# Kernel tuning notes

Hardware: AMD Instinct MI355X
Metric: run time of the kernel (lower is better)

Reference implementation:

```python
import jax, jax.numpy as jnp
import numpy as np

N_NODES = 100000
N_EDGES = 600000
D_IN = 128
D_OUT = 128

def gcn_conv(x, src, dst, W, b, n):
    # PyG GCNConv: h = X W; out_i = sum_j norm_ij * h_j + b, with self-loops and
    # symmetric normalization norm_ij = deg_i^{-1/2} deg_j^{-1/2}.
    deg = jax.ops.segment_sum(jnp.ones_like(dst, dtype=x.dtype), dst, num_segments=n)
    dinv = jnp.where(deg > 0, jax.lax.rsqrt(deg), 0.0)
    norm = dinv[src] * dinv[dst]            # [E]
    h = x @ W                                # [N, D_out]
    msg = h[src] * norm[:, None]             # gather + scale, [E, D_out]
    out = jax.ops.segment_sum(msg, dst, num_segments=n)
    return out + b

def setup_inputs() -> dict:
    key = jax.random.key(0)
    ks = jax.random.split(key, 8)
    x = jax.random.normal(ks[0], (N_NODES, D_IN), dtype=jnp.float32)
    edge_index = jax.random.randint(ks[1], (2, N_EDGES), 0, N_NODES, dtype=jnp.int64)
    s = (1.0 / np.sqrt(D_IN)).astype(np.float32) if isinstance(np.sqrt(D_IN), np.ndarray) else np.float32(1.0 / np.sqrt(D_IN))
    W1 = jax.random.normal(ks[2], (D_IN, D_OUT), dtype=jnp.float32) * s
    b1 = jnp.zeros((D_OUT,), dtype=jnp.float32)
    W2 = jax.random.normal(ks[3], (D_OUT, D_OUT), dtype=jnp.float32) * np.float32(1.0 / np.sqrt(D_OUT))
    b2 = jnp.zeros((D_OUT,), dtype=jnp.float32)
    Wfc = jax.random.normal(ks[4], (D_IN, D_OUT), dtype=jnp.float32) * s
    bfc = jnp.zeros((D_OUT,), dtype=jnp.float32)
    return {"x": x, "edge_index": edge_index, "W1": W1, "b1": b1,
            "W2": W2, "b2": b2, "Wfc": Wfc, "bfc": bfc}

def reference(x, edge_index, W1, b1, W2, b2, Wfc, bfc):
    n = x.shape[0]
    loop = jnp.arange(n, dtype=edge_index.dtype)
    src = jnp.concatenate([edge_index[0], loop])  # add self-loops
    dst = jnp.concatenate([edge_index[1], loop])
    res = x @ Wfc + bfc                           # linear residual branch
    h = jax.nn.relu(gcn_conv(x, src, dst, W1, b1, n))
    h = jax.nn.relu(gcn_conv(h, src, dst, W2, b2, n))
    return h + res
```

## Files before the change

### kernel.cpp

```cpp
#include <hip/hip_runtime.h>
#include <hip/hip_bf16.h>

#define D 128

typedef __bf16 bf16x8 __attribute__((ext_vector_type(8)));
typedef float f32x16 __attribute__((ext_vector_type(16)));

union U16 { uint4 u; bf16x8 v; };

static __device__ __forceinline__ unsigned short f2bf(float f) {
    unsigned u = __float_as_uint(f);
    unsigned r = (u + 0x7fffu + ((u >> 16) & 1u)) >> 16;
    return (unsigned short)r;
}
static __device__ __forceinline__ float bf2f(unsigned short s) {
    return __uint_as_float(((unsigned)s) << 16);
}
static __device__ __forceinline__ float u2f_lo(unsigned x) { return __uint_as_float(x << 16); }
static __device__ __forceinline__ float u2f_hi(unsigned x) { return __uint_as_float(x & 0xffff0000u); }

__global__ __launch_bounds__(256) void k_prep(
        const float* __restrict__ W1, const float* __restrict__ W2, const float* __restrict__ Wf,
        unsigned short* __restrict__ W1h, unsigned short* __restrict__ W1l,
        unsigned short* __restrict__ W2h, unsigned short* __restrict__ W2l,
        unsigned short* __restrict__ Wfh, unsigned short* __restrict__ Wfl,
        int* __restrict__ cnt, int n) {
    int idx = blockIdx.x * 256 + threadIdx.x;
    if (idx < 3 * 16384) {
        int which = idx >> 14;
        int local = idx & 16383;
        int k = local >> 7, c = local & 127;
        const float* W = (which == 0) ? W1 : (which == 1) ? W2 : Wf;
        unsigned short* Wh = (which == 0) ? W1h : (which == 1) ? W2h : Wfh;
        unsigned short* Wl = (which == 0) ? W1l : (which == 1) ? W2l : Wfl;
        float v = W[k * 128 + c];
        unsigned short h = f2bf(v);
        unsigned short l = f2bf(v - bf2f(h));
        Wh[c * 128 + k] = h;
        Wl[c * 128 + k] = l;
    }
    if (idx < n) cnt[idx] = 0;
}


__global__ __launch_bounds__(256) void k_hist(const int* __restrict__ dst,
                                              int* __restrict__ cnt, int e) {
    int i = blockIdx.x * 256 + threadIdx.x;
    if (i < e) atomicAdd(&cnt[dst[i]], 1);
}

#define SCAN_CHUNK 1024

__global__ __launch_bounds__(256) void k_scan_local(const int* __restrict__ cnt,
                                                    int* __restrict__ ptr,
                                                    int* __restrict__ sums, int n) {
    __shared__ int tsum[256];
    const int t = threadIdx.x;
    const int base = blockIdx.x * SCAN_CHUNK + t * 4;
    int v[4]; int s = 0;
    #pragma unroll
    for (int i = 0; i < 4; ++i) {
        int idx = base + i;
        v[i] = (idx < n) ? cnt[idx] : 0;
        s += v[i];
    }
    tsum[t] = s;
    __syncthreads();
    for (int off = 1; off < 256; off <<= 1) {
        int x = (t >= off) ? tsum[t - off] : 0;
        __syncthreads();
        tsum[t] += x;
        __syncthreads();
    }
    int run = (t > 0) ? tsum[t - 1] : 0;
    if (t == 255) sums[blockIdx.x] = tsum[255];
    #pragma unroll
    for (int i = 0; i < 4; ++i) {
        int idx = base + i;
        if (idx < n) ptr[idx] = run;
        run += v[i];
    }
}

__global__ __launch_bounds__(256) void k_scan_sums(int* __restrict__ sums, int nChunks) {
    __shared__ int ls[256];
    const int t = threadIdx.x;
    ls[t] = (t < nChunks) ? sums[t] : 0;
    __syncthreads();
    for (int off = 1; off < 256; off <<= 1) {
        int x = (t >= off) ? ls[t - off] : 0;
        __syncthreads();
        ls[t] += x;
        __syncthreads();
    }
    if (t < nChunks) sums[t] = (t > 0) ? ls[t - 1] : 0;
}

__global__ __launch_bounds__(256) void k_scan_add(int* __restrict__ ptr,
                                                  const int* __restrict__ sums,
                                                  int* __restrict__ cnt,
                                                  float* __restrict__ dinv,
                                                  int n, int e) {
    int i = blockIdx.x * 256 + threadIdx.x;
    if (i < n) {
        ptr[i] += sums[i >> 10];
        dinv[i] = rsqrtf((float)(1 + cnt[i]));
        cnt[i] = 0;
    }
    if (i == 0) ptr[n] = e;
}

__global__ __launch_bounds__(256) void k_fill(const int* __restrict__ src,
                                              const int* __restrict__ dst,
                                              const int* __restrict__ ptr,
                                              int* __restrict__ fill,
                                              int* __restrict__ csr_src, int e) {
    int i = blockIdx.x * 256 + threadIdx.x;
    if (i < e) {
        int d = dst[i];
        int slot = ptr[d] + atomicAdd(&fill[d], 1);
        csr_src[slot] = src[i];
    }
}

#define APAD 136

__global__ __launch_bounds__(256, 4) void k_gemm_rr(
        const float* __restrict__ A,
        const unsigned short* __restrict__ Bh, const unsigned short* __restrict__ Bl,
        const float* __restrict__ bias,
        unsigned short* __restrict__ outb,
        float* __restrict__ outf,
        int M, int nTiles) {
    __shared__ __align__(16) unsigned short As[2][32][APAD];

    const int tid = threadIdx.x;
    const int wave = tid >> 6;
    const int lane = tid & 63;
    const int l31 = lane & 31;
    const int quad8 = (lane >> 5) * 8;
    const int col = wave * 32 + l31;

    U16 bh[8], bl[8];
    #pragma unroll
    for (int ks = 0; ks < 8; ++ks) {
        const size_t bo = (size_t)col * D + ks * 16 + quad8;
        bh[ks].u = *(const uint4*)(Bh + bo);
        bl[ks].u = *(const uint4*)(Bl + bo);
    }
    const float bv = (bias != nullptr) ? bias[col] : 0.f;

    for (int t = blockIdx.x; t < nTiles; t += gridDim.x) {
        const int row0 = t * 32;

        #pragma unroll
        for (int i = 0; i < 4; ++i) {
            int f = tid + i * 256;
            int r = f >> 5, c4 = (f & 31) * 4;
            int rg = row0 + r; if (rg >= M) rg = M - 1;
            float4 v = *(const float4*)(A + (size_t)rg * D + c4);
            ushort4 hq, lq;
            hq.x = f2bf(v.x); hq.y = f2bf(v.y); hq.z = f2bf(v.z); hq.w = f2bf(v.w);
            lq.x = f2bf(v.x - bf2f(hq.x)); lq.y = f2bf(v.y - bf2f(hq.y));
            lq.z = f2bf(v.z - bf2f(hq.z)); lq.w = f2bf(v.w - bf2f(hq.w));
            *(ushort4*)&As[0][r][c4] = hq;
            *(ushort4*)&As[1][r][c4] = lq;
        }
        __syncthreads();

        f32x16 acc;
        #pragma unroll
        for (int r = 0; r < 16; ++r) acc[r] = 0.f;

        #pragma unroll
        for (int ks = 0; ks < 8; ++ks) {
            U16 ah, al;
            ah.u = *(const uint4*)&As[0][l31][ks * 16 + quad8];
            al.u = *(const uint4*)&As[1][l31][ks * 16 + quad8];
            acc = __builtin_amdgcn_mfma_f32_32x32x16_bf16(ah.v, bh[ks].v, acc, 0, 0, 0);
            acc = __builtin_amdgcn_mfma_f32_32x32x16_bf16(ah.v, bl[ks].v, acc, 0, 0, 0);
            acc = __builtin_amdgcn_mfma_f32_32x32x16_bf16(al.v, bh[ks].v, acc, 0, 0, 0);
        }
        __syncthreads();

        #pragma unroll
        for (int reg = 0; reg < 16; ++reg) {
            const int r = (reg & 3) + 8 * (reg >> 2) + 4 * (lane >> 5);
            const int rg = row0 + r;
            if (rg < M) {
                if (outb) outb[(size_t)rg * D + col] = f2bf(acc[reg]);
                else      outf[(size_t)rg * D + col] = acc[reg] + bv;
            }
        }
    }
}

__global__ __launch_bounds__(256, 4) void k_gemm_rr_bf(
        const unsigned short* __restrict__ A,
        const unsigned short* __restrict__ Bh, const unsigned short* __restrict__ Bl,
        unsigned short* __restrict__ outb,
        int M, int nTiles) {
    __shared__ __align__(16) unsigned short As[32][APAD];

    const int tid = threadIdx.x;
    const int wave = tid >> 6;
    const int lane = tid & 63;
    const int l31 = lane & 31;
    const int quad8 = (lane >> 5) * 8;
    const int col = wave * 32 + l31;

    U16 bh[8], bl[8];
    #pragma unroll
    for (int ks = 0; ks < 8; ++ks) {
        const size_t bo = (size_t)col * D + ks * 16 + quad8;
        bh[ks].u = *(const uint4*)(Bh + bo);
        bl[ks].u = *(const uint4*)(Bl + bo);
    }

    for (int t = blockIdx.x; t < nTiles; t += gridDim.x) {
        const int row0 = t * 32;

        #pragma unroll
        for (int i = 0; i < 2; ++i) {
            int f = tid + i * 256;
            int r = f >> 4, c8 = (f & 15) * 8;
            int rg = row0 + r; if (rg >= M) rg = M - 1;
            *(uint4*)&As[r][c8] = *(const uint4*)(A + (size_t)rg * D + c8);
        }
        __syncthreads();

        f32x16 acc;
        #pragma unroll
        for (int r = 0; r < 16; ++r) acc[r] = 0.f;

        #pragma unroll
        for (int ks = 0; ks < 8; ++ks) {
            U16 ah;
            ah.u = *(const uint4*)&As[l31][ks * 16 + quad8];
            acc = __builtin_amdgcn_mfma_f32_32x32x16_bf16(ah.v, bh[ks].v, acc, 0, 0, 0);
            acc = __builtin_amdgcn_mfma_f32_32x32x16_bf16(ah.v, bl[ks].v, acc, 0, 0, 0);
        }
        __syncthreads();

        #pragma unroll
        for (int reg = 0; reg < 16; ++reg) {
            const int r = (reg & 3) + 8 * (reg >> 2) + 4 * (lane >> 5);
            const int rg = row0 + r;
            if (rg < M) outb[(size_t)rg * D + col] = f2bf(acc[reg]);
        }
    }
}

__global__ __launch_bounds__(256) void k_gather_bf(const int* __restrict__ ptr,
                                                   const int* __restrict__ csr_src,
                                                   const float* __restrict__ dinv,
                                                   const unsigned short* __restrict__ h,
                                                   const float* __restrict__ bias,
                                                   const float* __restrict__ res,
                                                   float* __restrict__ outf,
                                                   unsigned short* __restrict__ outb,
                                                   int N) {
    const int g = threadIdx.x >> 5;
    const int lane = threadIdx.x & 31;
    const int i = blockIdx.x * 8 + g;
    if (i >= N) return;

    const int p0 = ptr[i];
    const int p1 = ptr[i + 1];
    const float di = dinv[i];

    float a0 = 0.f, a1 = 0.f, a2 = 0.f, a3 = 0.f;
    int j = p0;
    for (; j + 4 <= p1; j += 4) {
        const int s0 = csr_src[j + 0];
        const int s1 = csr_src[j + 1];
        const int s2 = csr_src[j + 2];
        const int s3 = csr_src[j + 3];
        const float c0 = dinv[s0], c1 = dinv[s1], c2 = dinv[s2], c3 = dinv[s3];
        const uint2 u0 = *(const uint2*)(h + (size_t)s0 * D + lane * 4);
        const uint2 u1 = *(const uint2*)(h + (size_t)s1 * D + lane * 4);
        const uint2 u2 = *(const uint2*)(h + (size_t)s2 * D + lane * 4);
        const uint2 u3 = *(const uint2*)(h + (size_t)s3 * D + lane * 4);
        a0 = fmaf(c0, u2f_lo(u0.x), a0); a1 = fmaf(c0, u2f_hi(u0.x), a1);
        a2 = fmaf(c0, u2f_lo(u0.y), a2); a3 = fmaf(c0, u2f_hi(u0.y), a3);
        a0 = fmaf(c1, u2f_lo(u1.x), a0); a1 = fmaf(c1, u2f_hi(u1.x), a1);
        a2 = fmaf(c1, u2f_lo(u1.y), a2); a3 = fmaf(c1, u2f_hi(u1.y), a3);
        a0 = fmaf(c2, u2f_lo(u2.x), a0); a1 = fmaf(c2, u2f_hi(u2.x), a1);
        a2 = fmaf(c2, u2f_lo(u2.y), a2); a3 = fmaf(c2, u2f_hi(u2.y), a3);
        a0 = fmaf(c3, u2f_lo(u3.x), a0); a1 = fmaf(c3, u2f_hi(u3.x), a1);
        a2 = fmaf(c3, u2f_lo(u3.y), a2); a3 = fmaf(c3, u2f_hi(u3.y), a3);
    }
    for (; j < p1; ++j) {
        const int s = csr_src[j];
        const float c = dinv[s];
        const uint2 u = *(const uint2*)(h + (size_t)s * D + lane * 4);
        a0 = fmaf(c, u2f_lo(u.x), a0);
        a1 = fmaf(c, u2f_hi(u.x), a1);
        a2 = fmaf(c, u2f_lo(u.y), a2);
        a3 = fmaf(c, u2f_hi(u.y), a3);
    }

    const uint2 us = *(const uint2*)(h + (size_t)i * D + lane * 4);
    const float4 bv = *(const float4*)(bias + lane * 4);
    const float self = di * di;
    float o0 = fmaxf(di * a0 + self * u2f_lo(us.x) + bv.x, 0.0f);
    float o1 = fmaxf(di * a1 + self * u2f_hi(us.x) + bv.y, 0.0f);
    float o2 = fmaxf(di * a2 + self * u2f_lo(us.y) + bv.z, 0.0f);
    float o3 = fmaxf(di * a3 + self * u2f_hi(us.y) + bv.w, 0.0f);
    if (outb) {
        ushort4 q = {f2bf(o0), f2bf(o1), f2bf(o2), f2bf(o3)};
        *(ushort4*)(outb + (size_t)i * D + lane * 4) = q;
    } else {
        if (res) {
            const float4 rv = *(const float4*)(res + (size_t)i * D + lane * 4);
            o0 += rv.x; o1 += rv.y; o2 += rv.z; o3 += rv.w;
        }
        float4 o = {o0, o1, o2, o3};
        *(float4*)(outf + (size_t)i * D + lane * 4) = o;
    }
}


extern "C" void kernel_launch(void* const* d_in, const int* in_sizes, int n_in,
                              void* d_out, int out_size, void* d_ws, size_t ws_size,
                              hipStream_t stream) {
    const int N = in_sizes[0] / D;
    const int E = in_sizes[1] / 2;

    const float* x   = (const float*)d_in[0];
    const int*   ei  = (const int*)d_in[1];
    const int*   src = ei;
    const int*   dst = ei + E;
    const float* W1  = (const float*)d_in[2];
    const float* b1  = (const float*)d_in[3];
    const float* W2  = (const float*)d_in[4];
    const float* b2  = (const float*)d_in[5];
    const float* Wfc = (const float*)d_in[6];
    const float* bfc = (const float*)d_in[7];
    float* out = (float*)d_out;

    char* ws = (char*)d_ws;
    size_t off = 0;
    auto alloc = [&](size_t bytes) { char* p = ws + off; off += (bytes + 255) & ~(size_t)255; return p; };
    float* dinv    = (float*)alloc((size_t)N * 4);
    int*   cnt     = (int*)  alloc((size_t)N * 4);
    int*   ptr     = (int*)  alloc((size_t)(N + 1) * 4);
    int*   sums    = (int*)  alloc(256 * 4);
    int*   csr_src = (int*)  alloc((size_t)E * 4);
    unsigned short* W1h = (unsigned short*)alloc(128 * 128 * 2);
    unsigned short* W1l = (unsigned short*)alloc(128 * 128 * 2);
    unsigned short* W2h = (unsigned short*)alloc(128 * 128 * 2);
    unsigned short* W2l = (unsigned short*)alloc(128 * 128 * 2);
    unsigned short* Wfh = (unsigned short*)alloc(128 * 128 * 2);
    unsigned short* Wfl = (unsigned short*)alloc(128 * 128 * 2);
    unsigned short* h    = (unsigned short*)alloc((size_t)N * D * 2);
    unsigned short* hb16 = (unsigned short*)alloc((size_t)N * D * 2);

    const int nBlk    = (N + 255) / 256;
    const int eBlk    = (E + 255) / 256;
    const int aBlk    = (N + 7) / 8;
    const int nChunks = (N + SCAN_CHUNK - 1) / SCAN_CHUNK;
    const int nTiles  = (N + 31) / 32;
    const int gBlk    = nTiles < 1024 ? nTiles : 1024;
    const int pBlk    = (nBlk > 192) ? nBlk : 192;

    k_prep<<<pBlk, 256, 0, stream>>>(W1, W2, Wfc, W1h, W1l, W2h, W2l, Wfh, Wfl, cnt, N);

    k_hist<<<eBlk, 256, 0, stream>>>(dst, cnt, E);
    k_scan_local<<<nChunks, 256, 0, stream>>>(cnt, ptr, sums, N);
    k_scan_sums<<<1, 256, 0, stream>>>(sums, nChunks);
    k_scan_add<<<nBlk, 256, 0, stream>>>(ptr, sums, cnt, dinv, N, E);
    k_fill<<<eBlk, 256, 0, stream>>>(src, dst, ptr, cnt, csr_src, E);

    k_gemm_rr<<<gBlk, 256, 0, stream>>>(x, W1h, W1l, nullptr, h, nullptr, N, nTiles);
    k_gemm_rr<<<gBlk, 256, 0, stream>>>(x, Wfh, Wfl, bfc, nullptr, out, N, nTiles);

    k_gather_bf<<<aBlk, 256, 0, stream>>>(ptr, csr_src, dinv, h, b1, nullptr, nullptr, hb16, N);

    k_gemm_rr_bf<<<gBlk, 256, 0, stream>>>(hb16, W2h, W2l, h, N, nTiles);

    k_gather_bf<<<aBlk, 256, 0, stream>>>(ptr, csr_src, dinv, h, b2, out, out, nullptr, N);
}
```

Baseline: 300.4 us.

## Pack CSR entries with source weights, pad rows to four, widen gather to wavefronts

The CSR array now stores (src, dinv[src]) pairs, and each row is padded to a multiple of four with zero-weight entries. This removes the dependent dinv gather and the scalar tail loop from the aggregation kernel. The gather now uses one 64-lane wavefront per node with two features per lane, and software-prefetches the next four edge records. The cost is a CSR buffer twice as wide plus padding, narrower per-lane loads, and a padding loop in the scan kernel.

```diff
diff --git a/kernel.cpp b/kernel.cpp
--- a/kernel.cpp
+++ b/kernel.cpp
@@ -61,7 +61,7 @@
     #pragma unroll
     for (int i = 0; i < 4; ++i) {
         int idx = base + i;
-        v[i] = (idx < n) ? cnt[idx] : 0;
+        v[i] = (idx < n) ? ((cnt[idx] + 3) & ~3) : 0;
         s += v[i];
     }
     tsum[t] = s;
@@ -100,26 +100,33 @@
                                                   const int* __restrict__ sums,
                                                   int* __restrict__ cnt,
                                                   float* __restrict__ dinv,
-                                                  int n, int e) {
+                                                  uint2* __restrict__ csr,
+                                                  int n) {
     int i = blockIdx.x * 256 + threadIdx.x;
     if (i < n) {
-        ptr[i] += sums[i >> 10];
-        dinv[i] = rsqrtf((float)(1 + cnt[i]));
+        const int c = cnt[i];
+        const int p = ptr[i] + sums[i >> 10];
+        ptr[i] = p;
+        dinv[i] = rsqrtf((float)(1 + c));
         cnt[i] = 0;
-    }
-    if (i == 0) ptr[n] = e;
+        const int pc = (c + 3) & ~3;
+        for (int j = p + c; j < p + pc; ++j) csr[j] = make_uint2(0u, 0u);
+        if (i == n - 1) ptr[n] = p + pc;
+    }
 }
 
 __global__ __launch_bounds__(256) void k_fill(const int* __restrict__ src,
                                               const int* __restrict__ dst,
                                               const int* __restrict__ ptr,
                                               int* __restrict__ fill,
-                                              int* __restrict__ csr_src, int e) {
+                                              const float* __restrict__ dinv,
+                                              uint2* __restrict__ csr, int e) {
     int i = blockIdx.x * 256 + threadIdx.x;
     if (i < e) {
         int d = dst[i];
+        int s = src[i];
         int slot = ptr[d] + atomicAdd(&fill[d], 1);
-        csr_src[slot] = src[i];
+        csr[slot] = make_uint2((unsigned)s, __float_as_uint(dinv[s]));
     }
 }
 
@@ -251,72 +258,69 @@
     }
 }
 
-__global__ __launch_bounds__(256) void k_gather_bf(const int* __restrict__ ptr,
-                                                   const int* __restrict__ csr_src,
-                                                   const float* __restrict__ dinv,
-                                                   const unsigned short* __restrict__ h,
-                                                   const float* __restrict__ bias,
-                                                   const float* __restrict__ res,
-                                                   float* __restrict__ outf,
-                                                   unsigned short* __restrict__ outb,
-                                                   int N) {
-    const int g = threadIdx.x >> 5;
-    const int lane = threadIdx.x & 31;
-    const int i = blockIdx.x * 8 + g;
+__global__ __launch_bounds__(256) void k_gather_w(const int* __restrict__ ptr,
+                                                  const uint2* __restrict__ csr,
+                                                  const float* __restrict__ dinv,
+                                                  const unsigned short* __restrict__ h,
+                                                  const float* __restrict__ bias,
+                                                  const float* __restrict__ res,
+                                                  float* __restrict__ outf,
+                                                  unsigned short* __restrict__ outb,
+                                                  int N) {
+    const int w = threadIdx.x >> 6;
+    const int lane = threadIdx.x & 63;
+    const int i = blockIdx.x * 4 + w;
     if (i >= N) return;
 
     const int p0 = ptr[i];
     const int p1 = ptr[i + 1];
     const float di = dinv[i];
-
-    float a0 = 0.f, a1 = 0.f, a2 = 0.f, a3 = 0.f;
+    const size_t lb = (size_t)(lane * 2);
+
+    float a0 = 0.f, a1 = 0.f;
+
     int j = p0;
-    for (; j + 4 <= p1; j += 4) {
-        const int s0 = csr_src[j + 0];
-        const int s1 = csr_src[j + 1];
-        const int s2 = csr_src[j + 2];
-        const int s3 = csr_src[j + 3];
-        const float c0 = dinv[s0], c1 = dinv[s1], c2 = dinv[s2], c3 = dinv[s3];
-        const uint2 u0 = *(const uint2*)(h + (size_t)s0 * D + lane * 4);
-        const uint2 u1 = *(const uint2*)(h + (size_t)s1 * D + lane * 4);
-        const uint2 u2 = *(const uint2*)(h + (size_t)s2 * D + lane * 4);
-        const uint2 u3 = *(const uint2*)(h + (size_t)s3 * D + lane * 4);
-        a0 = fmaf(c0, u2f_lo(u0.x), a0); a1 = fmaf(c0, u2f_hi(u0.x), a1);
-        a2 = fmaf(c0, u2f_lo(u0.y), a2); a3 = fmaf(c0, u2f_hi(u0.y), a3);
-        a0 = fmaf(c1, u2f_lo(u1.x), a0); a1 = fmaf(c1, u2f_hi(u1.x), a1);
-        a2 = fmaf(c1, u2f_lo(u1.y), a2); a3 = fmaf(c1, u2f_hi(u1.y), a3);
-        a0 = fmaf(c2, u2f_lo(u2.x), a0); a1 = fmaf(c2, u2f_hi(u2.x), a1);
-        a2 = fmaf(c2, u2f_lo(u2.y), a2); a3 = fmaf(c2, u2f_hi(u2.y), a3);
-        a0 = fmaf(c3, u2f_lo(u3.x), a0); a1 = fmaf(c3, u2f_hi(u3.x), a1);
-        a2 = fmaf(c3, u2f_lo(u3.y), a2); a3 = fmaf(c3, u2f_hi(u3.y), a3);
-    }
-    for (; j < p1; ++j) {
-        const int s = csr_src[j];
-        const float c = dinv[s];
-        const uint2 u = *(const uint2*)(h + (size_t)s * D + lane * 4);
-        a0 = fmaf(c, u2f_lo(u.x), a0);
-        a1 = fmaf(c, u2f_hi(u.x), a1);
-        a2 = fmaf(c, u2f_lo(u.y), a2);
-        a3 = fmaf(c, u2f_hi(u.y), a3);
-    }
-
-    const uint2 us = *(const uint2*)(h + (size_t)i * D + lane * 4);
-    const float4 bv = *(const float4*)(bias + lane * 4);
+    if (j < p1) {
+        const unsigned* cb = (const unsigned*)csr;
+        uint4 e0 = *(const uint4*)(cb + 2 * (size_t)j);
+        uint4 e1 = *(const uint4*)(cb + 2 * (size_t)j + 4);
+        while (1) {
+            const int jn = j + 4;
+            const bool more = (jn < p1);
+            uint4 f0, f1;
+            if (more) {
+                f0 = *(const uint4*)(cb + 2 * (size_t)jn);
+                f1 = *(const uint4*)(cb + 2 * (size_t)jn + 4);
+            }
+            const unsigned u0 = *(const unsigned*)(h + (size_t)e0.x * D + lb);
+            const unsigned u1 = *(const unsigned*)(h + (size_t)e0.z * D + lb);
+            const unsigned u2 = *(const unsigned*)(h + (size_t)e1.x * D + lb);
+            const unsigned u3 = *(const unsigned*)(h + (size_t)e1.z * D + lb);
+            const float w0 = __uint_as_float(e0.y);
+            const float w1 = __uint_as_float(e0.w);
+            const float w2 = __uint_as_float(e1.y);
+            const float w3 = __uint_as_float(e1.w);
+            a0 = fmaf(w0, u2f_lo(u0), a0); a1 = fmaf(w0, u2f_hi(u0), a1);
+            a0 = fmaf(w1, u2f_lo(u1), a0); a1 = fmaf(w1, u2f_hi(u1), a1);
+            a0 = fmaf(w2, u2f_lo(u2), a0); a1 = fmaf(w2, u2f_hi(u2), a1);
+            a0 = fmaf(w3, u2f_lo(u3), a0); a1 = fmaf(w3, u2f_hi(u3), a1);
+            if (!more) break;
+            e0 = f0; e1 = f1; j = jn;
+        }
+    }
+
+    const unsigned us = *(const unsigned*)(h + (size_t)i * D + lb);
+    const float2 bv = *(const float2*)(bias + lane * 2);
     const float self = di * di;
-    float o0 = fmaxf(di * a0 + self * u2f_lo(us.x) + bv.x, 0.0f);
-    float o1 = fmaxf(di * a1 + self * u2f_hi(us.x) + bv.y, 0.0f);
-    float o2 = fmaxf(di * a2 + self * u2f_lo(us.y) + bv.z, 0.0f);
-    float o3 = fmaxf(di * a3 + self * u2f_hi(us.y) + bv.w, 0.0f);
+    float o0 = fmaxf(di * a0 + self * u2f_lo(us) + bv.x, 0.0f);
+    float o1 = fmaxf(di * a1 + self * u2f_hi(us) + bv.y, 0.0f);
     if (outb) {
-        ushort4 q = {f2bf(o0), f2bf(o1), f2bf(o2), f2bf(o3)};
-        *(ushort4*)(outb + (size_t)i * D + lane * 4) = q;
+        ushort2 q = {f2bf(o0), f2bf(o1)};
+        *(ushort2*)(outb + (size_t)i * D + lane * 2) = q;
     } else {
-        if (res) {
-            const float4 rv = *(const float4*)(res + (size_t)i * D + lane * 4);
-            o0 += rv.x; o1 += rv.y; o2 += rv.z; o3 += rv.w;
-        }
-        float4 o = {o0, o1, o2, o3};
-        *(float4*)(outf + (size_t)i * D + lane * 4) = o;
+        const float2 rv = *(const float2*)(res + (size_t)i * D + lane * 2);
+        float2 o = {o0 + rv.x, o1 + rv.y};
+        *(float2*)(outf + (size_t)i * D + lane * 2) = o;
     }
 }
 
@@ -346,7 +350,7 @@
     int*   cnt     = (int*)  alloc((size_t)N * 4);
     int*   ptr     = (int*)  alloc((size_t)(N + 1) * 4);
     int*   sums    = (int*)  alloc(256 * 4);
-    int*   csr_src = (int*)  alloc((size_t)E * 4);
+    uint2* csr     = (uint2*)alloc((size_t)(E + 3 * N + 64) * sizeof(uint2));
     unsigned short* W1h = (unsigned short*)alloc(128 * 128 * 2);
     unsigned short* W1l = (unsigned short*)alloc(128 * 128 * 2);
     unsigned short* W2h = (unsigned short*)alloc(128 * 128 * 2);
@@ -358,7 +362,7 @@
 
     const int nBlk    = (N + 255) / 256;
     const int eBlk    = (E + 255) / 256;
-    const int aBlk    = (N + 7) / 8;
+    const int aBlk    = (N + 3) / 4;
     const int nChunks = (N + SCAN_CHUNK - 1) / SCAN_CHUNK;
     const int nTiles  = (N + 31) / 32;
     const int gBlk    = nTiles < 1024 ? nTiles : 1024;
@@ -369,15 +373,15 @@
     k_hist<<<eBlk, 256, 0, stream>>>(dst, cnt, E);
     k_scan_local<<<nChunks, 256, 0, stream>>>(cnt, ptr, sums, N);
     k_scan_sums<<<1, 256, 0, stream>>>(sums, nChunks);
-    k_scan_add<<<nBlk, 256, 0, stream>>>(ptr, sums, cnt, dinv, N, E);
-    k_fill<<<eBlk, 256, 0, stream>>>(src, dst, ptr, cnt, csr_src, E);
+    k_scan_add<<<nBlk, 256, 0, stream>>>(ptr, sums, cnt, dinv, csr, N);
+    k_fill<<<eBlk, 256, 0, stream>>>(src, dst, ptr, cnt, dinv, csr, E);
 
     k_gemm_rr<<<gBlk, 256, 0, stream>>>(x, W1h, W1l, nullptr, h, nullptr, N, nTiles);
     k_gemm_rr<<<gBlk, 256, 0, stream>>>(x, Wfh, Wfl, bfc, nullptr, out, N, nTiles);
 
-    k_gather_bf<<<aBlk, 256, 0, stream>>>(ptr, csr_src, dinv, h, b1, nullptr, nullptr, hb16, N);
+    k_gather_w<<<aBlk, 256, 0, stream>>>(ptr, csr, dinv, h, b1, nullptr, nullptr, hb16, N);
 
     k_gemm_rr_bf<<<gBlk, 256, 0, stream>>>(hb16, W2h, W2l, h, N, nTiles);
 
-    k_gather_bf<<<aBlk, 256, 0, stream>>>(ptr, csr_src, dinv, h, b2, out, out, nullptr, N);
-}
+    k_gather_w<<<aBlk, 256, 0, stream>>>(ptr, csr, dinv, h, b2, out, out, nullptr, N);
+}
```

Result: slower. 307.0 us (+2.2%).

## Fuse x GEMMs into dual kernel and pack edge weights into CSR

Applied to the files above, without the earlier changes.

Merges the two GEMMs that read x (layer-1 weight and residual linear) into one kernel computing both outputs from a shared A tile. Stores dinv of the source next to the source index in the CSR during fill, removing a dependent random load per edge in both gather passes. In exchange, the dual GEMM holds four weight fragment sets in registers and is limited to lower occupancy, and the CSR doubles in size.

```diff
diff --git a/kernel.cpp b/kernel.cpp
--- a/kernel.cpp
+++ b/kernel.cpp
@@ -114,23 +114,26 @@
                                               const int* __restrict__ dst,
                                               const int* __restrict__ ptr,
                                               int* __restrict__ fill,
-                                              int* __restrict__ csr_src, int e) {
+                                              const float* __restrict__ dinv,
+                                              uint2* __restrict__ csr, int e) {
     int i = blockIdx.x * 256 + threadIdx.x;
     if (i < e) {
         int d = dst[i];
+        int s = src[i];
         int slot = ptr[d] + atomicAdd(&fill[d], 1);
-        csr_src[slot] = src[i];
+        csr[slot] = make_uint2((unsigned)s, __float_as_uint(dinv[s]));
     }
 }
 
 #define APAD 136
 
-__global__ __launch_bounds__(256, 4) void k_gemm_rr(
+__global__ __launch_bounds__(256, 2) void k_gemm_dual(
         const float* __restrict__ A,
-        const unsigned short* __restrict__ Bh, const unsigned short* __restrict__ Bl,
-        const float* __restrict__ bias,
-        unsigned short* __restrict__ outb,
-        float* __restrict__ outf,
+        const unsigned short* __restrict__ B1h, const unsigned short* __restrict__ B1l,
+        const unsigned short* __restrict__ B2h, const unsigned short* __restrict__ B2l,
+        const float* __restrict__ bias2,
+        unsigned short* __restrict__ out1,
+        float* __restrict__ out2,
         int M, int nTiles) {
     __shared__ __align__(16) unsigned short As[2][32][APAD];
 
@@ -141,14 +144,16 @@
     const int quad8 = (lane >> 5) * 8;
     const int col = wave * 32 + l31;
 
-    U16 bh[8], bl[8];
+    U16 b1h[8], b1l[8], b2h[8], b2l[8];
     #pragma unroll
     for (int ks = 0; ks < 8; ++ks) {
         const size_t bo = (size_t)col * D + ks * 16 + quad8;
-        bh[ks].u = *(const uint4*)(Bh + bo);
-        bl[ks].u = *(const uint4*)(Bl + bo);
-    }
-    const float bv = (bias != nullptr) ? bias[col] : 0.f;
+        b1h[ks].u = *(const uint4*)(B1h + bo);
+        b1l[ks].u = *(const uint4*)(B1l + bo);
+        b2h[ks].u = *(const uint4*)(B2h + bo);
+        b2l[ks].u = *(const uint4*)(B2l + bo);
+    }
+    const float bv = bias2[col];
 
     for (int t = blockIdx.x; t < nTiles; t += gridDim.x) {
         const int row0 = t * 32;
@@ -168,18 +173,21 @@
         }
         __syncthreads();
 
-        f32x16 acc;
-        #pragma unroll
-        for (int r = 0; r < 16; ++r) acc[r] = 0.f;
+        f32x16 acc1, acc2;
+        #pragma unroll
+        for (int r = 0; r < 16; ++r) { acc1[r] = 0.f; acc2[r] = 0.f; }
 
         #pragma unroll
         for (int ks = 0; ks < 8; ++ks) {
             U16 ah, al;
             ah.u = *(const uint4*)&As[0][l31][ks * 16 + quad8];
             al.u = *(const uint4*)&As[1][l31][ks * 16 + quad8];
-            acc = __builtin_amdgcn_mfma_f32_32x32x16_bf16(ah.v, bh[ks].v, acc, 0, 0, 0);
-            acc = __builtin_amdgcn_mfma_f32_32x32x16_bf16(ah.v, bl[ks].v, acc, 0, 0, 0);
-            acc = __builtin_amdgcn_mfma_f32_32x32x16_bf16(al.v, bh[ks].v, acc, 0, 0, 0);
+            acc1 = __builtin_amdgcn_mfma_f32_32x32x16_bf16(ah.v, b1h[ks].v, acc1, 0, 0, 0);
+            acc2 = __builtin_amdgcn_mfma_f32_32x32x16_bf16(ah.v, b2h[ks].v, acc2, 0, 0, 0);
+            acc1 = __builtin_amdgcn_mfma_f32_32x32x16_bf16(ah.v, b1l[ks].v, acc1, 0, 0, 0);
+            acc2 = __builtin_amdgcn_mfma_f32_32x32x16_bf16(ah.v, b2l[ks].v, acc2, 0, 0, 0);
+            acc1 = __builtin_amdgcn_mfma_f32_32x32x16_bf16(al.v, b1h[ks].v, acc1, 0, 0, 0);
+            acc2 = __builtin_amdgcn_mfma_f32_32x32x16_bf16(al.v, b2h[ks].v, acc2, 0, 0, 0);
         }
         __syncthreads();
 
@@ -188,8 +196,8 @@
             const int r = (reg & 3) + 8 * (reg >> 2) + 4 * (lane >> 5);
             const int rg = row0 + r;
             if (rg < M) {
-                if (outb) outb[(size_t)rg * D + col] = f2bf(acc[reg]);
-                else      outf[(size_t)rg * D + col] = acc[reg] + bv;
+                out1[(size_t)rg * D + col] = f2bf(acc1[reg]);
+                out2[(size_t)rg * D + col] = acc2[reg] + bv;
             }
         }
     }
@@ -251,15 +259,15 @@
     }
 }
 
-__global__ __launch_bounds__(256) void k_gather_bf(const int* __restrict__ ptr,
-                                                   const int* __restrict__ csr_src,
-                                                   const float* __restrict__ dinv,
-                                                   const unsigned short* __restrict__ h,
-                                                   const float* __restrict__ bias,
-                                                   const float* __restrict__ res,
-                                                   float* __restrict__ outf,
-                                                   unsigned short* __restrict__ outb,
-                                                   int N) {
+__global__ __launch_bounds__(256) void k_gather_w(const int* __restrict__ ptr,
+                                                  const uint2* __restrict__ csr,
+                                                  const float* __restrict__ dinv,
+                                                  const unsigned short* __restrict__ h,
+                                                  const float* __restrict__ bias,
+                                                  const float* __restrict__ res,
+                                                  float* __restrict__ outf,
+                                                  unsigned short* __restrict__ outb,
+                                                  int N) {
     const int g = threadIdx.x >> 5;
     const int lane = threadIdx.x & 31;
     const int i = blockIdx.x * 8 + g;
@@ -270,17 +278,19 @@
     const float di = dinv[i];
 
     float a0 = 0.f, a1 = 0.f, a2 = 0.f, a3 = 0.f;
+    const unsigned* cb = (const unsigned*)csr;
     int j = p0;
     for (; j + 4 <= p1; j += 4) {
-        const int s0 = csr_src[j + 0];
-        const int s1 = csr_src[j + 1];
-        const int s2 = csr_src[j + 2];
-        const int s3 = csr_src[j + 3];
-        const float c0 = dinv[s0], c1 = dinv[s1], c2 = dinv[s2], c3 = dinv[s3];
-        const uint2 u0 = *(const uint2*)(h + (size_t)s0 * D + lane * 4);
-        const uint2 u1 = *(const uint2*)(h + (size_t)s1 * D + lane * 4);
-        const uint2 u2 = *(const uint2*)(h + (size_t)s2 * D + lane * 4);
-        const uint2 u3 = *(const uint2*)(h + (size_t)s3 * D + lane * 4);
+        const uint4 e0 = *(const uint4*)(cb + 2 * (size_t)j);
+        const uint4 e1 = *(const uint4*)(cb + 2 * (size_t)j + 4);
+        const float c0 = __uint_as_float(e0.y);
+        const float c1 = __uint_as_float(e0.w);
+        const float c2 = __uint_as_float(e1.y);
+        const float c3 = __uint_as_float(e1.w);
+        const uint2 u0 = *(const uint2*)(h + (size_t)e0.x * D + lane * 4);
+        const uint2 u1 = *(const uint2*)(h + (size_t)e0.z * D + lane * 4);
+        const uint2 u2 = *(const uint2*)(h + (size_t)e1.x * D + lane * 4);
+        const uint2 u3 = *(const uint2*)(h + (size_t)e1.z * D + lane * 4);
         a0 = fmaf(c0, u2f_lo(u0.x), a0); a1 = fmaf(c0, u2f_hi(u0.x), a1);
         a2 = fmaf(c0, u2f_lo(u0.y), a2); a3 = fmaf(c0, u2f_hi(u0.y), a3);
         a0 = fmaf(c1, u2f_lo(u1.x), a0); a1 = fmaf(c1, u2f_hi(u1.x), a1);
@@ -291,9 +301,9 @@
         a2 = fmaf(c3, u2f_lo(u3.y), a2); a3 = fmaf(c3, u2f_hi(u3.y), a3);
     }
     for (; j < p1; ++j) {
-        const int s = csr_src[j];
-        const float c = dinv[s];
-        const uint2 u = *(const uint2*)(h + (size_t)s * D + lane * 4);
+        const uint2 e = csr[j];
+        const float c = __uint_as_float(e.y);
+        const uint2 u = *(const uint2*)(h + (size_t)e.x * D + lane * 4);
         a0 = fmaf(c, u2f_lo(u.x), a0);
         a1 = fmaf(c, u2f_hi(u.x), a1);
         a2 = fmaf(c, u2f_lo(u.y), a2);
@@ -311,11 +321,8 @@
         ushort4 q = {f2bf(o0), f2bf(o1), f2bf(o2), f2bf(o3)};
         *(ushort4*)(outb + (size_t)i * D + lane * 4) = q;
     } else {
-        if (res) {
-            const float4 rv = *(const float4*)(res + (size_t)i * D + lane * 4);
-            o0 += rv.x; o1 += rv.y; o2 += rv.z; o3 += rv.w;
-        }
-        float4 o = {o0, o1, o2, o3};
+        const float4 rv = *(const float4*)(res + (size_t)i * D + lane * 4);
+        float4 o = {o0 + rv.x, o1 + rv.y, o2 + rv.z, o3 + rv.w};
         *(float4*)(outf + (size_t)i * D + lane * 4) = o;
     }
 }
@@ -346,7 +353,7 @@
     int*   cnt     = (int*)  alloc((size_t)N * 4);
     int*   ptr     = (int*)  alloc((size_t)(N + 1) * 4);
     int*   sums    = (int*)  alloc(256 * 4);
-    int*   csr_src = (int*)  alloc((size_t)E * 4);
+    uint2* csr     = (uint2*)alloc((size_t)(E + 64) * sizeof(uint2));
     unsigned short* W1h = (unsigned short*)alloc(128 * 128 * 2);
     unsigned short* W1l = (unsigned short*)alloc(128 * 128 * 2);
     unsigned short* W2h = (unsigned short*)alloc(128 * 128 * 2);
@@ -370,14 +377,13 @@
     k_scan_local<<<nChunks, 256, 0, stream>>>(cnt, ptr, sums, N);
     k_scan_sums<<<1, 256, 0, stream>>>(sums, nChunks);
     k_scan_add<<<nBlk, 256, 0, stream>>>(ptr, sums, cnt, dinv, N, E);
-    k_fill<<<eBlk, 256, 0, stream>>>(src, dst, ptr, cnt, csr_src, E);
-
-    k_gemm_rr<<<gBlk, 256, 0, stream>>>(x, W1h, W1l, nullptr, h, nullptr, N, nTiles);
-    k_gemm_rr<<<gBlk, 256, 0, stream>>>(x, Wfh, Wfl, bfc, nullptr, out, N, nTiles);
-
-    k_gather_bf<<<aBlk, 256, 0, stream>>>(ptr, csr_src, dinv, h, b1, nullptr, nullptr, hb16, N);
+    k_fill<<<eBlk, 256, 0, stream>>>(src, dst, ptr, cnt, dinv, csr, E);
+
+    k_gemm_dual<<<gBlk, 256, 0, stream>>>(x, W1h, W1l, Wfh, Wfl, bfc, h, out, N, nTiles);
+
+    k_gather_w<<<aBlk, 256, 0, stream>>>(ptr, csr, dinv, h, b1, nullptr, nullptr, hb16, N);
 
     k_gemm_rr_bf<<<gBlk, 256, 0, stream>>>(hb16, W2h, W2l, h, N, nTiles);
 
-    k_gather_bf<<<aBlk, 256, 0, stream>>>(ptr, csr_src, dinv, h, b2, out, out, nullptr, N);
-}
+    k_gather_w<<<aBlk, 256, 0, stream>>>(ptr, csr, dinv, h, b2, out, out, nullptr, N);
+}
```

Measured after the change: 294.6 us. Within noise of the previous version (-1.9%).
